# Kernel optimization log

Hardware: AMD Instinct MI355X
Metric: run time of the kernel (lower is better)

## Reference

```python
import jax, jax.numpy as jnp
import numpy as np

N = 100000      # nodes
E = 1000000     # edges per layer
D_IN, D_H, D_OUT = 128, 128, 64


def setup_inputs() -> dict:
    key = jax.random.key(0)
    ks = jax.random.split(key, 8)
    x = jax.random.normal(ks[0], (N, D_IN), dtype=jnp.float32)
    edge_index1 = jax.random.randint(ks[1], (2, E), 0, N)
    edge_index2 = jax.random.randint(ks[2], (2, E), 0, N)

    def w(k, fan_in, fan_out):
        return jax.random.normal(k, (fan_in, fan_out), dtype=jnp.float32) / np.sqrt(fan_in).astype(np.float32)

    return {
        "x": x,
        "edge_index1": edge_index1,
        "edge_index2": edge_index2,
        "W_l1": w(ks[3], D_IN, D_H),
        "b_l1": jnp.zeros((D_H,), jnp.float32),
        "W_r1": w(ks[4], D_IN, D_H),
        "W_l2": w(ks[5], D_H, D_OUT),
        "b_l2": jnp.zeros((D_OUT,), jnp.float32),
        "W_r2": w(ks[6], D_H, D_OUT),
    }


def _sage_conv(x, edge_index, W_l, b_l, W_r):
    """PyG SAGEConv, aggr='mean', normalize=False, root_weight=True.
    out = lin_l(mean_{j->i} x_j) + lin_r(x_i). lin_r has no bias."""
    src, dst = edge_index[0], edge_index[1]
    n = x.shape[0]
    msg_sum = jax.ops.segment_sum(x[src], dst, num_segments=n)            # [N, d]
    cnt = jax.ops.segment_sum(jnp.ones((edge_index.shape[1],), x.dtype), dst, num_segments=n)
    agg = msg_sum / jnp.maximum(cnt, 1.0)[:, None]                        # mean over in-edges
    return agg @ W_l + b_l + x @ W_r


def reference(x, edge_index1, edge_index2, W_l1, b_l1, W_r1, W_l2, b_l2, W_r2):
    h = jax.nn.relu(_sage_conv(x, edge_index1, W_l1, b_l1, W_r1))  # dropout off in eval
    h = _sage_conv(h, edge_index2, W_l2, b_l2, W_r2)
    return jax.nn.log_softmax(h, axis=-1).astype(jnp.float32)     # output_type='logit'
```

## Files before the change

### kernel.cpp

```cpp
#include <hip/hip_runtime.h>
#include <hip/hip_bf16.h>


typedef __attribute__((ext_vector_type(8))) short bf16x8;
typedef __attribute__((ext_vector_type(4))) float f32x4;
typedef unsigned int u32;
typedef unsigned short u16;

constexpr int BSHIFT = 9;
constexpr int BNODES = 1 << BSHIFT;
constexpr int CHUNK  = 4096;
constexpr int EPT    = CHUNK / 256;

__device__ __forceinline__ u16 f2bf(float f) {
    u32 u = __float_as_uint(f);
    return (u16)((u + 0x7fffu + ((u >> 16) & 1u)) >> 16);
}
__device__ __forceinline__ float blo(u32 u) { return __uint_as_float(u << 16); }
__device__ __forceinline__ float bhi(u32 u) { return __uint_as_float(u & 0xffff0000u); }
__device__ __forceinline__ void accp(float2& a, u32 u) { a.x += blo(u); a.y += bhi(u); }
__device__ __forceinline__ u32 pack2(float x, float y) {
    return (u32)f2bf(x) | ((u32)f2bf(y) << 16);
}


__device__ __forceinline__ void pack_body(int bid,
                                          const float* __restrict__ Wl1, const float* __restrict__ Wr1,
                                          const float* __restrict__ Wl2, const float* __restrict__ Wr2,
                                          u16* __restrict__ Pl1, u16* __restrict__ Pr1,
                                          u16* __restrict__ Pl2, u16* __restrict__ Pr2) {
    int u = bid * 256 + threadIdx.x;
    if (u >= 6144) return;
    const float* W; u16* P; int O;
    if (u < 2048)      { W = Wl1; P = Pl1; O = 128; }
    else if (u < 4096) { W = Wr1; P = Pr1; O = 128; u -= 2048; }
    else if (u < 5120) { W = Wl2; P = Pl2; O = 64;  u -= 4096; }
    else               { W = Wr2; P = Pr2; O = 64;  u -= 5120; }
    int lane = u & 63, t = u >> 6;
    int ntiles = O / 16;
    int ks = t / ntiles, nt = t % ntiles;
    int k0 = ks * 32 + (lane >> 4) * 8;
    int col = nt * 16 + (lane & 15);
    bf16x8 o;
#pragma unroll
    for (int j = 0; j < 8; ++j) o[j] = (short)f2bf(W[(size_t)(k0 + j) * O + col]);
    *reinterpret_cast<bf16x8*>(P + (size_t)u * 8) = o;
}

__device__ __forceinline__ void count_body(int b, const int* __restrict__ ei, int E,
                                           int nB, int* __restrict__ bcnt, int* lcnt) {
    for (int i = threadIdx.x; i < nB; i += 256) lcnt[i] = 0;
    __syncthreads();
    const int base = b * CHUNK;
    const int end = min(base + CHUNK, E);
    for (int e = base + (int)threadIdx.x; e < end; e += 256)
        atomicAdd(&lcnt[ei[E + e] >> BSHIFT], 1);
    __syncthreads();
    for (int i = threadIdx.x; i < nB; i += 256)
        if (lcnt[i]) atomicAdd(&bcnt[i], lcnt[i]);
}

__device__ __forceinline__ void partition_body(int b, const int* __restrict__ ei, int E,
                                               int* __restrict__ bcur, u32* __restrict__ ebuf,
                                               int nB, int* lds) {
    int* lcnt = lds;
    int* lbase = lds + 1024;
    for (int i = threadIdx.x; i < nB; i += 256) lcnt[i] = 0;
    __syncthreads();
    const int base = b * CHUNK;

    u32 pk[EPT]; int bk[EPT];
#pragma unroll
    for (int k = 0; k < EPT; ++k) {
        int e = base + (int)threadIdx.x + k * 256;
        if (e < E) {
            int s = ei[e], d = ei[E + e];
            bk[k] = d >> BSHIFT;
            pk[k] = ((u32)(d & (BNODES - 1)) << 23) | (u32)s;
            atomicAdd(&lcnt[bk[k]], 1);
        } else bk[k] = -1;
    }
    __syncthreads();
    for (int i = threadIdx.x; i < nB; i += 256) {
        int c = lcnt[i];
        lbase[i] = c ? atomicAdd(&bcur[i], c) : 0;
        lcnt[i] = 0;
    }
    __syncthreads();
#pragma unroll
    for (int k = 0; k < EPT; ++k) {
        if (bk[k] >= 0) {
            int p = lbase[bk[k]] + atomicAdd(&lcnt[bk[k]], 1);
            ebuf[p] = pk[k];
        }
    }
}

__device__ __forceinline__ void build_body(int bkt, const u32* __restrict__ ebuf,
                                           const int* __restrict__ bbase, int n,
                                           int* __restrict__ rowptr, int* __restrict__ csr,
                                           int* lds) {
    int* hist   = lds;
    int* sstart = lds + BNODES;
    int* spart  = lds + 2 * BNODES;
    const int bb = bbase[bkt], be = bbase[bkt + 1];
    const int node0 = bkt << BSHIFT;

    for (int i = threadIdx.x; i < BNODES; i += 256) hist[i] = 0;
    __syncthreads();
    for (int e = bb + (int)threadIdx.x; e < be; e += 256)
        atomicAdd(&hist[ebuf[e] >> 23], 1);
    __syncthreads();

    const int t = threadIdx.x;
    const int v0 = hist[2 * t], v1 = hist[2 * t + 1];
    const int ts = v0 + v1;
    const int lane = t & 63, wave = t >> 6;
    int x = ts;
#pragma unroll
    for (int off = 1; off < 64; off <<= 1) { int y = __shfl_up(x, off); if (lane >= off) x += y; }
    if (lane == 63) spart[wave] = x;
    __syncthreads();
    int woff = 0;
#pragma unroll
    for (int w = 0; w < 4; ++w) if (w < wave) woff += spart[w];
    const int excl = woff + x - ts;
    sstart[2 * t] = excl;
    sstart[2 * t + 1] = excl + v0;
    const int nd0 = node0 + 2 * t, nd1 = node0 + 2 * t + 1;
    if (nd0 < n) rowptr[nd0] = bb + excl;
    if (nd1 < n) rowptr[nd1] = bb + excl + v0;
    for (int i = threadIdx.x; i < BNODES; i += 256) hist[i] = 0;
    __syncthreads();

    for (int e = bb + (int)threadIdx.x; e < be; e += 256) {
        u32 pkv = ebuf[e];
        int dl = pkv >> 23;
        int p = atomicAdd(&hist[dl], 1);
        csr[bb + sstart[dl] + p] = (int)(pkv & 0x7FFFFFu);
    }
}

__device__ __forceinline__ void gemm1_body(int bid, const float* __restrict__ x,
                                           const u16* __restrict__ Py, const u16* __restrict__ Pz,
                                           const float* __restrict__ bias,
                                           u16* __restrict__ yb, u16* __restrict__ zb,
                                           int n, u16* WB ) {
    constexpr int STR = 136;
    {
        const uint4* s1 = reinterpret_cast<const uint4*>(Py);
        const uint4* s2 = reinterpret_cast<const uint4*>(Pz);
        uint4* dst = reinterpret_cast<uint4*>(WB);
        for (int i = threadIdx.x; i < 2048; i += 256) dst[i] = s1[i];
        for (int i = threadIdx.x; i < 2048; i += 256) dst[2048 + i] = s2[i];
    }
    __syncthreads();

    const int wave = threadIdx.x >> 6, lane = threadIdx.x & 63;
    const int row0 = bid * 64 + wave * 16;
    const int lr = lane & 15, lg = lane >> 4;
    const bool active = row0 < n;

    f32x4 accy[8], accz[8];
#pragma unroll
    for (int t = 0; t < 8; ++t) { accy[t] = (f32x4){0,0,0,0}; accz[t] = (f32x4){0,0,0,0}; }

    if (active) {
        const int ra = min(row0 + lr, n - 1);
        const float* Ar = x + (size_t)ra * 128;
        float4 A0[4], A1[4];
#pragma unroll
        for (int ks = 0; ks < 4; ++ks) {
            A0[ks] = *reinterpret_cast<const float4*>(Ar + (ks * 4 + lg) * 8);
            A1[ks] = *reinterpret_cast<const float4*>(Ar + (ks * 4 + lg) * 8 + 4);
        }
        const bf16x8* YL = reinterpret_cast<const bf16x8*>(WB) + lane;
        const bf16x8* ZL = YL + 2048;
#pragma unroll
        for (int ks = 0; ks < 4; ++ks) {
            bf16x8 a;
            a[0] = (short)f2bf(A0[ks].x); a[1] = (short)f2bf(A0[ks].y);
            a[2] = (short)f2bf(A0[ks].z); a[3] = (short)f2bf(A0[ks].w);
            a[4] = (short)f2bf(A1[ks].x); a[5] = (short)f2bf(A1[ks].y);
            a[6] = (short)f2bf(A1[ks].z); a[7] = (short)f2bf(A1[ks].w);
#pragma unroll
            for (int t = 0; t < 8; ++t) {
                accy[t] = __builtin_amdgcn_mfma_f32_16x16x32_bf16(a, YL[(ks * 8 + t) * 64], accy[t], 0, 0, 0);
                accz[t] = __builtin_amdgcn_mfma_f32_16x16x32_bf16(a, ZL[(ks * 8 + t) * 64], accz[t], 0, 0, 0);
            }
        }
    }
    __syncthreads();

    if (!active) return;
    u16* L = WB + wave * 16 * STR;
#pragma unroll
    for (int t = 0; t < 8; ++t)
#pragma unroll
        for (int r = 0; r < 4; ++r)
            L[(lg * 4 + r) * STR + t * 16 + lr] = f2bf(accy[t][r]);
#pragma unroll
    for (int it = 0; it < 4; ++it) {
        int idx = it * 64 + lane;
        int row = idx >> 4, c8 = idx & 15;
        if (row0 + row < n)
            *reinterpret_cast<uint4*>(yb + (size_t)(row0 + row) * 128 + c8 * 8) =
                *reinterpret_cast<const uint4*>(&L[row * STR + c8 * 8]);
    }
#pragma unroll
    for (int t = 0; t < 8; ++t) {
        float bv = bias[t * 16 + lr];
#pragma unroll
        for (int r = 0; r < 4; ++r)
            L[(lg * 4 + r) * STR + t * 16 + lr] = f2bf(accz[t][r] + bv);
    }
#pragma unroll
    for (int it = 0; it < 4; ++it) {
        int idx = it * 64 + lane;
        int row = idx >> 4, c8 = idx & 15;
        if (row0 + row < n)
            *reinterpret_cast<uint4*>(zb + (size_t)(row0 + row) * 128 + c8 * 8) =
                *reinterpret_cast<const uint4*>(&L[row * STR + c8 * 8]);
    }
}


__global__ __launch_bounds__(256) void pack_count(const float* __restrict__ Wl1, const float* __restrict__ Wr1,
                                                  const float* __restrict__ Wl2, const float* __restrict__ Wr2,
                                                  u16* __restrict__ Pl1, u16* __restrict__ Pr1,
                                                  u16* __restrict__ Pl2, u16* __restrict__ Pr2,
                                                  const int* __restrict__ ei1, int E1, int ng1, int* __restrict__ bc1,
                                                  const int* __restrict__ ei2, int E2, int* __restrict__ bc2, int nB) {
    __shared__ int lcnt[1024];
    const int b = blockIdx.x;
    if (b < 24) {
        pack_body(b, Wl1, Wr1, Wl2, Wr2, Pl1, Pr1, Pl2, Pr2);
    } else {
        int c = b - 24;
        if (c < ng1) count_body(c, ei1, E1, nB, bc1, lcnt);
        else         count_body(c - ng1, ei2, E2, nB, bc2, lcnt);
    }
}

__global__ void bucket_scan_both(const int* __restrict__ bc1, int* __restrict__ bbase1,
                                 int* __restrict__ bcur1, int* __restrict__ rp1, int E1,
                                 const int* __restrict__ bc2, int* __restrict__ bbase2,
                                 int* __restrict__ bcur2, int* __restrict__ rp2, int E2,
                                 int nB, int n) {
    const int* bcnt; int* bbase; int* bcur; int* rowptr; int E;
    if (blockIdx.x == 0) { bcnt = bc1; bbase = bbase1; bcur = bcur1; rowptr = rp1; E = E1; }
    else                 { bcnt = bc2; bbase = bbase2; bcur = bcur2; rowptr = rp2; E = E2; }
    const int lane = threadIdx.x;
    int run = 0;
    for (int r = 0; r < nB; r += 64) {
        int i = r + lane;
        int v = (i < nB) ? bcnt[i] : 0;
        int x = v;
#pragma unroll
        for (int off = 1; off < 64; off <<= 1) { int y = __shfl_up(x, off); if (lane >= off) x += y; }
        int excl = run + x - v;
        if (i < nB) { bbase[i] = excl; bcur[i] = excl; }
        run += __shfl(x, 63);
    }
    if (lane == 0) { bbase[nB] = run; rowptr[n] = E; }
}

__global__ __launch_bounds__(256) void partition_both(const int* __restrict__ ei1, int E1, int ng1,
                                                      int* __restrict__ bcur1, u32* __restrict__ eb1,
                                                      const int* __restrict__ ei2, int E2,
                                                      int* __restrict__ bcur2, u32* __restrict__ eb2,
                                                      int nB) {
    __shared__ int lds[2048];
    const int b = blockIdx.x;
    if (b < ng1) partition_body(b, ei1, E1, bcur1, eb1, nB, lds);
    else         partition_body(b - ng1, ei2, E2, bcur2, eb2, nB, lds);
}

__global__ __launch_bounds__(256) void build_gemm1(const u32* __restrict__ eb1,
                                                   const int* __restrict__ bbase1,
                                                   int* __restrict__ rp1, int* __restrict__ csr1,
                                                   const u32* __restrict__ eb2,
                                                   const int* __restrict__ bbase2,
                                                   int* __restrict__ rp2, int* __restrict__ csr2,
                                                   int nB, int n,
                                                   const float* __restrict__ x,
                                                   const u16* __restrict__ Py, const u16* __restrict__ Pz,
                                                   const float* __restrict__ bias,
                                                   u16* __restrict__ yb, u16* __restrict__ zb) {
    __shared__ __align__(16) u16 WB[32768];
    const int b = blockIdx.x;
    if (b < nB)           build_body(b, eb1, bbase1, n, rp1, csr1, (int*)WB);
    else if (b < 2 * nB)  build_body(b - nB, eb2, bbase2, n, rp2, csr2, (int*)WB);
    else                  gemm1_body(b - 2 * nB, x, Py, Pz, bias, yb, zb, n, WB);
}

__global__ __launch_bounds__(256) void gather_gemm2(const u16* __restrict__ y1,
                                                    const int* __restrict__ rp1,
                                                    const int* __restrict__ csr1,
                                                    const u16* __restrict__ z1,
                                                    const u16* __restrict__ Pl2,
                                                    const u16* __restrict__ Pr2,
                                                    const float* __restrict__ bias,
                                                    u16* __restrict__ y2, u16* __restrict__ z2,
                                                    int n) {
    constexpr int STR = 136;
    __shared__ __align__(16) u16 H[4][16 * STR];
    const int wave = threadIdx.x >> 6, lane = threadIdx.x & 63;
    const int l = lane & 15, g = lane >> 4;
    const int nb0 = blockIdx.x * 64 + wave * 16;
    if (nb0 >= n) return;
    u16* Hw = H[wave];

    for (int r = 0; r < 4; ++r) {
        const int lrow = r * 4 + g;
        const int node = nb0 + lrow;
        uint4 o = {0u, 0u, 0u, 0u};
        if (node < n) {
            const int start = rp1[node], end = rp1[node + 1];
            float2 a0 = {0,0}, a1 = {0,0}, a2 = {0,0}, a3 = {0,0};
            int e = start;
            for (; e + 4 <= end; e += 4) {
                const int s0 = csr1[e], s1 = csr1[e + 1], s2 = csr1[e + 2], s3 = csr1[e + 3];
                uint4 v0 = *reinterpret_cast<const uint4*>(y1 + (size_t)s0 * 128 + l * 8);
                uint4 v1 = *reinterpret_cast<const uint4*>(y1 + (size_t)s1 * 128 + l * 8);
                uint4 v2 = *reinterpret_cast<const uint4*>(y1 + (size_t)s2 * 128 + l * 8);
                uint4 v3 = *reinterpret_cast<const uint4*>(y1 + (size_t)s3 * 128 + l * 8);
                accp(a0, v0.x); accp(a1, v0.y); accp(a2, v0.z); accp(a3, v0.w);
                accp(a0, v1.x); accp(a1, v1.y); accp(a2, v1.z); accp(a3, v1.w);
                accp(a0, v2.x); accp(a1, v2.y); accp(a2, v2.z); accp(a3, v2.w);
                accp(a0, v3.x); accp(a1, v3.y); accp(a2, v3.z); accp(a3, v3.w);
            }
            for (; e < end; ++e) {
                const int s0 = csr1[e];
                uint4 v0 = *reinterpret_cast<const uint4*>(y1 + (size_t)s0 * 128 + l * 8);
                accp(a0, v0.x); accp(a1, v0.y); accp(a2, v0.z); accp(a3, v0.w);
            }
            const float inv = 1.0f / fmaxf((float)(end - start), 1.0f);
            uint4 zr = *reinterpret_cast<const uint4*>(z1 + (size_t)node * 128 + l * 8);
            o.x = pack2(fmaxf(a0.x * inv + blo(zr.x), 0.f), fmaxf(a0.y * inv + bhi(zr.x), 0.f));
            o.y = pack2(fmaxf(a1.x * inv + blo(zr.y), 0.f), fmaxf(a1.y * inv + bhi(zr.y), 0.f));
            o.z = pack2(fmaxf(a2.x * inv + blo(zr.z), 0.f), fmaxf(a2.y * inv + bhi(zr.z), 0.f));
            o.w = pack2(fmaxf(a3.x * inv + blo(zr.w), 0.f), fmaxf(a3.y * inv + bhi(zr.w), 0.f));
        }
        *reinterpret_cast<uint4*>(&Hw[lrow * STR + l * 8]) = o;
    }

    const bf16x8* Y8 = reinterpret_cast<const bf16x8*>(Pl2) + lane;
    const bf16x8* Z8 = reinterpret_cast<const bf16x8*>(Pr2) + lane;
    f32x4 ay[4], az[4];
#pragma unroll
    for (int t = 0; t < 4; ++t) { ay[t] = (f32x4){0,0,0,0}; az[t] = (f32x4){0,0,0,0}; }
#pragma unroll
    for (int ks = 0; ks < 4; ++ks) {
        bf16x8 a = *reinterpret_cast<const bf16x8*>(&Hw[l * STR + ks * 32 + g * 8]);
#pragma unroll
        for (int t = 0; t < 4; ++t) {
            ay[t] = __builtin_amdgcn_mfma_f32_16x16x32_bf16(a, Y8[(size_t)(ks * 4 + t) * 64], ay[t], 0, 0, 0);
            az[t] = __builtin_amdgcn_mfma_f32_16x16x32_bf16(a, Z8[(size_t)(ks * 4 + t) * 64], az[t], 0, 0, 0);
        }
    }

#pragma unroll
    for (int t = 0; t < 4; ++t)
#pragma unroll
        for (int r = 0; r < 4; ++r)
            Hw[(g * 4 + r) * STR + t * 16 + l] = f2bf(ay[t][r]);
#pragma unroll
    for (int it = 0; it < 2; ++it) {
        int idx = it * 64 + lane, row = idx >> 3, c8 = idx & 7;
        if (nb0 + row < n)
            *reinterpret_cast<uint4*>(y2 + (size_t)(nb0 + row) * 64 + c8 * 8) =
                *reinterpret_cast<const uint4*>(&Hw[row * STR + c8 * 8]);
    }
#pragma unroll
    for (int t = 0; t < 4; ++t) {
        float bv = bias[t * 16 + l];
#pragma unroll
        for (int r = 0; r < 4; ++r)
            Hw[(g * 4 + r) * STR + t * 16 + l] = f2bf(az[t][r] + bv);
    }
#pragma unroll
    for (int it = 0; it < 2; ++it) {
        int idx = it * 64 + lane, row = idx >> 3, c8 = idx & 7;
        if (nb0 + row < n)
            *reinterpret_cast<uint4*>(z2 + (size_t)(nb0 + row) * 64 + c8 * 8) =
                *reinterpret_cast<const uint4*>(&Hw[row * STR + c8 * 8]);
    }
}

__global__ __launch_bounds__(256) void gather_lsm(const u16* __restrict__ y,
                                                  const int* __restrict__ rowptr,
                                                  const int* __restrict__ csr,
                                                  const u16* __restrict__ z,
                                                  float* __restrict__ out, int n) {
    const int wave = threadIdx.x >> 6, lane = threadIdx.x & 63;
    const int l = lane & 7, g = lane >> 3;
    const int node = (blockIdx.x * 4 + wave) * 8 + g;
    const bool ok = node < n;
    int start = 0, end = 0;
    if (ok) { start = rowptr[node]; end = rowptr[node + 1]; }

    float2 a0 = {0,0}, a1 = {0,0}, a2 = {0,0}, a3 = {0,0};
    int e = start;
    for (; e + 4 <= end; e += 4) {
        const int s0 = csr[e], s1 = csr[e + 1], s2 = csr[e + 2], s3 = csr[e + 3];
        uint4 v0 = *reinterpret_cast<const uint4*>(y + (size_t)s0 * 64 + l * 8);
        uint4 v1 = *reinterpret_cast<const uint4*>(y + (size_t)s1 * 64 + l * 8);
        uint4 v2 = *reinterpret_cast<const uint4*>(y + (size_t)s2 * 64 + l * 8);
        uint4 v3 = *reinterpret_cast<const uint4*>(y + (size_t)s3 * 64 + l * 8);
        accp(a0, v0.x); accp(a1, v0.y); accp(a2, v0.z); accp(a3, v0.w);
        accp(a0, v1.x); accp(a1, v1.y); accp(a2, v1.z); accp(a3, v1.w);
        accp(a0, v2.x); accp(a1, v2.y); accp(a2, v2.z); accp(a3, v2.w);
        accp(a0, v3.x); accp(a1, v3.y); accp(a2, v3.z); accp(a3, v3.w);
    }
    for (; e < end; ++e) {
        const int s0 = csr[e];
        uint4 v0 = *reinterpret_cast<const uint4*>(y + (size_t)s0 * 64 + l * 8);
        accp(a0, v0.x); accp(a1, v0.y); accp(a2, v0.z); accp(a3, v0.w);
    }

    if (ok) {
        const float inv = 1.0f / fmaxf((float)(end - start), 1.0f);
        uint4 zr = *reinterpret_cast<const uint4*>(z + (size_t)node * 64 + l * 8);
        float v0 = a0.x * inv + blo(zr.x), v1 = a0.y * inv + bhi(zr.x);
        float v2 = a1.x * inv + blo(zr.y), v3 = a1.y * inv + bhi(zr.y);
        float v4 = a2.x * inv + blo(zr.z), v5 = a2.y * inv + bhi(zr.z);
        float v6 = a3.x * inv + blo(zr.w), v7 = a3.y * inv + bhi(zr.w);

        float m = fmaxf(fmaxf(fmaxf(v0, v1), fmaxf(v2, v3)), fmaxf(fmaxf(v4, v5), fmaxf(v6, v7)));
        m = fmaxf(m, __shfl_xor(m, 1));
        m = fmaxf(m, __shfl_xor(m, 2));
        m = fmaxf(m, __shfl_xor(m, 4));
        float s = expf(v0 - m) + expf(v1 - m) + expf(v2 - m) + expf(v3 - m) +
                  expf(v4 - m) + expf(v5 - m) + expf(v6 - m) + expf(v7 - m);
        s += __shfl_xor(s, 1);
        s += __shfl_xor(s, 2);
        s += __shfl_xor(s, 4);
        const float c = m + logf(s);
        float* op = out + (size_t)node * 64 + l * 8;
        *reinterpret_cast<float4*>(op)     = (float4){v0 - c, v1 - c, v2 - c, v3 - c};
        *reinterpret_cast<float4*>(op + 4) = (float4){v4 - c, v5 - c, v6 - c, v7 - c};
    }
}

extern "C" void kernel_launch(void* const* d_in, const int* in_sizes, int n_in,
                              void* d_out, int out_size, void* d_ws, size_t ws_size,
                              hipStream_t stream) {
    const float* x    = (const float*)d_in[0];
    const int*   ei1  = (const int*)d_in[1];
    const int*   ei2  = (const int*)d_in[2];
    const float* W_l1 = (const float*)d_in[3];
    const float* b_l1 = (const float*)d_in[4];
    const float* W_r1 = (const float*)d_in[5];
    const float* W_l2 = (const float*)d_in[6];
    const float* b_l2 = (const float*)d_in[7];
    const float* W_r2 = (const float*)d_in[8];

    const int n  = in_sizes[0] / 128;
    const int E1 = in_sizes[1] / 2;
    const int E2 = in_sizes[2] / 2;
    const int nB = (n + BNODES - 1) >> BSHIFT;
    const int ng1 = (E1 + CHUNK - 1) / CHUNK;
    const int ng2 = (E2 + CHUNK - 1) / CHUNK;
    const int ngp = ng1 + ng2;

    char* w = (char*)d_ws;
    u16* yb  = (u16*)w; w += (size_t)n * 128 * 2;
    u16* zb  = (u16*)w; w += (size_t)n * 128 * 2;
    u16* y2b = (u16*)w; w += (size_t)n * 64 * 2;
    u16* z2b = (u16*)w; w += (size_t)n * 64 * 2;
    u16* Pl1 = (u16*)w; w += 16384 * 2;
    u16* Pr1 = (u16*)w; w += 16384 * 2;
    u16* Pl2 = (u16*)w; w += 8192 * 2;
    u16* Pr2 = (u16*)w; w += 8192 * 2;
    int* rp1   = (int*)w; w += (size_t)(n + 1) * 4;
    int* rp2   = (int*)w; w += (size_t)(n + 1) * 4;
    int* bcnt  = (int*)w; w += 2048 * 4;
    int* bbase1= (int*)w; w += 1025 * 4;
    int* bbase2= (int*)w; w += 1025 * 4;
    int* bcur1 = (int*)w; w += 1024 * 4;
    int* bcur2 = (int*)w; w += 1024 * 4;
    int* csr1  = (int*)w; w += (size_t)E1 * 4;
    int* csr2  = (int*)w; w += (size_t)E2 * 4;
    u32* eb1   = (u32*)w; w += (size_t)E1 * 4;
    u32* eb2   = (u32*)w;

    const int gb64 = (n + 63) / 64;

    hipMemsetAsync(bcnt, 0, 2048 * sizeof(int), stream);

    pack_count<<<24 + ngp, 256, 0, stream>>>(W_l1, W_r1, W_l2, W_r2, Pl1, Pr1, Pl2, Pr2,
                                             ei1, E1, ng1, bcnt, ei2, E2, bcnt + 1024, nB);
    bucket_scan_both<<<2, 64, 0, stream>>>(bcnt, bbase1, bcur1, rp1, E1,
                                           bcnt + 1024, bbase2, bcur2, rp2, E2, nB, n);
    partition_both<<<ngp, 256, 0, stream>>>(ei1, E1, ng1, bcur1, eb1,
                                            ei2, E2, bcur2, eb2, nB);
    build_gemm1<<<2 * nB + gb64, 256, 0, stream>>>(eb1, bbase1, rp1, csr1,
                                                   eb2, bbase2, rp2, csr2, nB, n,
                                                   x, Pl1, Pr1, b_l1, yb, zb);
    gather_gemm2<<<gb64, 256, 0, stream>>>(yb, rp1, csr1, zb, Pl2, Pr2, b_l2, y2b, z2b, n);
    gather_lsm<<<(n + 31) / 32, 256, 0, stream>>>(y2b, rp2, csr2, z2b, (float*)d_out, n);
}
```

Measured before the change: 171.0 us.

## Restructure gather_gemm2 to one gather row per wave group and split MFMA tiles across waves

Each 512-thread block now handles 32 nodes, with each wave gathering just 4 nodes in a single pass instead of looping over 16 nodes per wave. The second-layer GEMM is then shared across the 8 waves: each wave computes 2 of the 16 output 16x16 tiles from a block-shared LDS tile, and every thread writes out in one pass. This exposes more independent gathers at once to hide memory latency and spreads the MFMA work more evenly. In exchange it adds block-wide barriers and loads fewer B fragments per wave per k-step, which lowers reuse of each A fragment.

Result: faster. 163.7 us (-4.2%).

```diff
diff --git a/kernel.cpp b/kernel.cpp
--- a/kernel.cpp
+++ b/kernel.cpp
@@ -294,7 +294,7 @@
     else                  gemm1_body(b - 2 * nB, x, Py, Pz, bias, yb, zb, n, WB);
 }
 
-__global__ __launch_bounds__(256) void gather_gemm2(const u16* __restrict__ y1,
+__global__ __launch_bounds__(512) void gather_gemm2(const u16* __restrict__ y1,
                                                     const int* __restrict__ rp1,
                                                     const int* __restrict__ csr1,
                                                     const u16* __restrict__ z1,
@@ -304,16 +304,14 @@
                                                     u16* __restrict__ y2, u16* __restrict__ z2,
                                                     int n) {
     constexpr int STR = 136;
-    __shared__ __align__(16) u16 H[4][16 * STR];
-    const int wave = threadIdx.x >> 6, lane = threadIdx.x & 63;
-    const int l = lane & 15, g = lane >> 4;
-    const int nb0 = blockIdx.x * 64 + wave * 16;
-    if (nb0 >= n) return;
-    u16* Hw = H[wave];
-
-    for (int r = 0; r < 4; ++r) {
-        const int lrow = r * 4 + g;
-        const int node = nb0 + lrow;
+    __shared__ __align__(16) u16 H[32 * STR];
+    const int wid = threadIdx.x >> 6, lane = threadIdx.x & 63;
+    const int node0 = blockIdx.x * 32;
+
+    {
+        const int l = lane & 15, g = lane >> 4;
+        const int lrow = wid * 4 + g;
+        const int node = node0 + lrow;
         uint4 o = {0u, 0u, 0u, 0u};
         if (node < n) {
             const int start = rp1[node], end = rp1[node + 1];
@@ -342,49 +340,47 @@
             o.z = pack2(fmaxf(a2.x * inv + blo(zr.z), 0.f), fmaxf(a2.y * inv + bhi(zr.z), 0.f));
             o.w = pack2(fmaxf(a3.x * inv + blo(zr.w), 0.f), fmaxf(a3.y * inv + bhi(zr.w), 0.f));
         }
-        *reinterpret_cast<uint4*>(&Hw[lrow * STR + l * 8]) = o;
-    }
-
-    const bf16x8* Y8 = reinterpret_cast<const bf16x8*>(Pl2) + lane;
-    const bf16x8* Z8 = reinterpret_cast<const bf16x8*>(Pr2) + lane;
-    f32x4 ay[4], az[4];
-#pragma unroll
-    for (int t = 0; t < 4; ++t) { ay[t] = (f32x4){0,0,0,0}; az[t] = (f32x4){0,0,0,0}; }
-#pragma unroll
-    for (int ks = 0; ks < 4; ++ks) {
-        bf16x8 a = *reinterpret_cast<const bf16x8*>(&Hw[l * STR + ks * 32 + g * 8]);
-#pragma unroll
-        for (int t = 0; t < 4; ++t) {
-            ay[t] = __builtin_amdgcn_mfma_f32_16x16x32_bf16(a, Y8[(size_t)(ks * 4 + t) * 64], ay[t], 0, 0, 0);
-            az[t] = __builtin_amdgcn_mfma_f32_16x16x32_bf16(a, Z8[(size_t)(ks * 4 + t) * 64], az[t], 0, 0, 0);
+        *reinterpret_cast<uint4*>(&H[lrow * STR + l * 8]) = o;
+    }
+    __syncthreads();
+
+    const int l = lane & 15, g = lane >> 4;
+    f32x4 acc[2];
+    int km[2], kc[2], kr[2];
+#pragma unroll
+    for (int i = 0; i < 2; ++i) {
+        const int k = wid * 2 + i;
+        km[i] = k & 1; kc[i] = (k >> 1) & 3; kr[i] = k >> 3;
+        acc[i] = (f32x4){0, 0, 0, 0};
+        const u16* P = km[i] ? Pr2 : Pl2;
+        const bf16x8* B8 = reinterpret_cast<const bf16x8*>(P) + lane;
+#pragma unroll
+        for (int ks = 0; ks < 4; ++ks) {
+            bf16x8 a = *reinterpret_cast<const bf16x8*>(&H[(kr[i] * 16 + l) * STR + ks * 32 + g * 8]);
+            acc[i] = __builtin_amdgcn_mfma_f32_16x16x32_bf16(a, B8[(size_t)(ks * 4 + kc[i]) * 64], acc[i], 0, 0, 0);
         }
     }
-
-#pragma unroll
-    for (int t = 0; t < 4; ++t)
-#pragma unroll
-        for (int r = 0; r < 4; ++r)
-            Hw[(g * 4 + r) * STR + t * 16 + l] = f2bf(ay[t][r]);
-#pragma unroll
-    for (int it = 0; it < 2; ++it) {
-        int idx = it * 64 + lane, row = idx >> 3, c8 = idx & 7;
-        if (nb0 + row < n)
-            *reinterpret_cast<uint4*>(y2 + (size_t)(nb0 + row) * 64 + c8 * 8) =
-                *reinterpret_cast<const uint4*>(&Hw[row * STR + c8 * 8]);
-    }
-#pragma unroll
-    for (int t = 0; t < 4; ++t) {
-        float bv = bias[t * 16 + l];
-#pragma unroll
-        for (int r = 0; r < 4; ++r)
-            Hw[(g * 4 + r) * STR + t * 16 + l] = f2bf(az[t][r] + bv);
-    }
-#pragma unroll
-    for (int it = 0; it < 2; ++it) {
-        int idx = it * 64 + lane, row = idx >> 3, c8 = idx & 7;
-        if (nb0 + row < n)
-            *reinterpret_cast<uint4*>(z2 + (size_t)(nb0 + row) * 64 + c8 * 8) =
-                *reinterpret_cast<const uint4*>(&Hw[row * STR + c8 * 8]);
+    __syncthreads();
+
+#pragma unroll
+    for (int i = 0; i < 2; ++i) {
+        const float bv = km[i] ? bias[kc[i] * 16 + l] : 0.f;
+#pragma unroll
+        for (int j = 0; j < 4; ++j)
+            H[(kr[i] * 16 + g * 4 + j) * STR + km[i] * 64 + kc[i] * 16 + l] = f2bf(acc[i][j] + bv);
+    }
+    __syncthreads();
+
+    {
+        const int t = threadIdx.x;
+        const int m = t >> 8;
+        const int idx = t & 255;
+        const int row = idx >> 3, c8 = idx & 7;
+        if (node0 + row < n) {
+            u16* dst = m ? z2 : y2;
+            *reinterpret_cast<uint4*>(dst + (size_t)(node0 + row) * 64 + c8 * 8) =
+                *reinterpret_cast<const uint4*>(&H[row * STR + m * 64 + c8 * 8]);
+        }
     }
 }
 
@@ -498,6 +494,7 @@
     build_gemm1<<<2 * nB + gb64, 256, 0, stream>>>(eb1, bbase1, rp1, csr1,
                                                    eb2, bbase2, rp2, csr2, nB, n,
                                                    x, Pl1, Pr1, b_l1, yb, zb);
-    gather_gemm2<<<gb64, 256, 0, stream>>>(yb, rp1, csr1, zb, Pl2, Pr2, b_l2, y2b, z2b, n);
+    gather_gemm2<<<(n + 31) / 32, 512, 0, stream>>>(yb, rp1, csr1, zb, Pl2, Pr2, b_l2,
+                                                    y2b, z2b, n);
     gather_lsm<<<(n + 31) / 32, 256, 0, stream>>>(y2b, rp2, csr2, z2b, (float*)d_out, n);
 }
```
